# Optimization experiments

Measured on AMD Instinct MI355X. Metric: run time of the kernel, lower is better.

## Reference

```python
import jax, jax.numpy as jnp
import numpy as np

LMAX = 3
NBASIS = 10
MAX_RADIUS = 10.0
NUM_GRAPHS = 1024
N_NODES = 50000
Z_DIM = 16
SH_DIM = (LMAX + 1) ** 2  # 16
SMOOTH_FINITE_C = 1.14136  # e3nn normalization constant for smooth_finite basis


def spherical_harmonics_l3(vec):
    """e3nn real spherical harmonics, lmax=3, normalize=True, normalization='component'.
    vec: [N,3] -> [N,16]."""
    r = jnp.linalg.norm(vec, axis=-1, keepdims=True)
    u = vec / r
    x, y, z = u[..., 0], u[..., 1], u[..., 2]
    one = jnp.ones_like(x)
    s3, s5, s7, s15 = np.sqrt(3.0), np.sqrt(5.0), np.sqrt(7.0), np.sqrt(15.0)
    x2, y2, z2 = x * x, y * y, z * z
    x2z2 = x2 + z2
    # l = 2 (e3nn generated polynomials, component normalization)
    sh2_0 = s15 * x * z
    sh2_1 = s15 * x * y
    sh2_2 = s5 * (y2 - 0.5 * x2z2)
    sh2_3 = s15 * y * z
    sh2_4 = (s15 / 2.0) * (z2 - x2)
    # l = 3
    c42_6 = np.sqrt(42.0) / 6.0
    c168_8 = np.sqrt(168.0) / 8.0
    sh3_0 = c42_6 * (sh2_0 * z + sh2_4 * x)
    sh3_1 = s7 * sh2_0 * y
    sh3_2 = c168_8 * (4.0 * y2 - x2z2) * x
    sh3_3 = (s7 / 2.0) * y * (2.0 * y2 - 3.0 * x2z2)
    sh3_4 = c168_8 * z * (4.0 * y2 - x2z2)
    sh3_5 = s7 * sh2_4 * y
    sh3_6 = c42_6 * (sh2_4 * z - sh2_0 * x)
    return jnp.stack([
        one,
        s3 * x, s3 * y, s3 * z,
        sh2_0, sh2_1, sh2_2, sh2_3, sh2_4,
        sh3_0, sh3_1, sh3_2, sh3_3, sh3_4, sh3_5, sh3_6,
    ], axis=-1)


def soft_one_hot_smooth_finite(d):
    """e3nn soft_one_hot_linspace(basis='smooth_finite', cutoff=True). d: [N] -> [N, NBASIS]."""
    values = jnp.linspace(0.0, MAX_RADIUS, NBASIS + 2)[1:-1]  # interior points
    step = MAX_RADIUS / (NBASIS + 1)
    diff = (d[:, None] - values) / step

    def soft_unit_step(u):
        safe = jnp.where(u > 0.0, u, 1.0)
        return jnp.where(u > 0.0, jnp.exp(-1.0 / safe), 0.0)

    c = SMOOTH_FINITE_C * np.exp(2.0)
    return c * soft_unit_step(diff + 1.0) * soft_unit_step(1.0 - diff)


def setup_inputs() -> dict:
    key = jax.random.key(0)
    k1, k2, k3 = jax.random.split(key, 3)
    x = jax.random.uniform(k1, (N_NODES, Z_DIM), dtype=jnp.float32)
    pos = jax.random.normal(k2, (N_NODES, 3), dtype=jnp.float32)
    batch = jnp.sort(jax.random.randint(k3, (N_NODES,), 0, NUM_GRAPHS, dtype=jnp.int64))
    return {"x": x, "pos": pos, "batch": batch}


def reference(x, pos, batch):
    edge_vec = pos
    edge_length = jnp.linalg.norm(edge_vec, axis=1)
    # radial embedding, scaled by sqrt(number_of_basis)
    basis = soft_one_hot_smooth_finite(edge_length) * np.sqrt(NBASIS)  # [N, B]
    sh = spherical_harmonics_l3(edge_vec)  # [N, 16]
    # FullTensorProduct(Zx0e, sh) then FullTensorProduct(., Bx0e):
    # scalar x irrep paths reduce to exact elementwise products (component norm),
    # with e3nn layout per l-block: [z, b, m] flattened, blocks concatenated over l.
    n = x.shape[0]
    sh_slices = [(0, 1), (1, 4), (4, 9), (9, 16)]  # l = 0..3
    blocks = []
    for lo, hi in sh_slices:
        blk = jnp.einsum('nz,nb,nm->nzbm', x, basis, sh[:, lo:hi])
        blocks.append(blk.reshape(n, -1))
    feats = jnp.concatenate(blocks, axis=-1)  # [N, Z*B*16]
    # scatter mean over graphs
    seg_sum = jax.ops.segment_sum(feats, batch, num_segments=NUM_GRAPHS)
    cnt = jax.ops.segment_sum(jnp.ones((n, 1), dtype=feats.dtype), batch, num_segments=NUM_GRAPHS)
    return seg_sum / jnp.maximum(cnt, 1.0)
```

## Files before the change

kernel.cpp:

```cpp
#include <hip/hip_runtime.h>
#include <cmath>

#define NGRAPHS 1024
#define ZDIM 16
#define NB 10
#define SHD 16
#define FEAT 2560
#define CHUNK 96
#define CSTRIDE 132
#define WIN 1536

__global__ __launch_bounds__(256) void yfe_kernel(
    const float* __restrict__ xin,
    const float* __restrict__ pos,
    const int* __restrict__ batch,
    float* __restrict__ out,
    int n_nodes)
{
    const int g = blockIdx.x;
    const int tid = threadIdx.x;
    const int n = n_nodes;

    __shared__ int s_red[12];
    __shared__ int s_cnt[2][9];
    __shared__ __align__(16) float s_xT[ZDIM][CSTRIDE];
    __shared__ __align__(16) float s_shA[SHD][CSTRIDE];
    __shared__ __align__(16) float s_shB[SHD][CSTRIDE];
    __shared__ __align__(16) float s_out[FEAT];

    int start, end;
    bool window_ok = (n >= WIN);
    if (window_ok) {
        const int ctr = (int)(((long long)(2 * g + 1) * n) >> 11);
        int p0 = ctr - WIN / 2;
        if (p0 < 0) p0 = 0;
        if (p0 > n - WIN) p0 = n - WIN;
        int vals[6];
#pragma unroll
        for (int k = 0; k < 6; ++k) vals[k] = batch[p0 + tid + k * 256];
        int wA = 0, wB = 0;
#pragma unroll
        for (int k = 0; k < 6; ++k) {
            wA += __popcll(__ballot(vals[k] < g));
            wB += __popcll(__ballot(vals[k] < g + 1));
        }
        if ((tid & 63) == 0) {
            s_red[tid >> 6]       = wA;
            s_red[4 + (tid >> 6)] = wB;
        }
        if (tid == 0)   s_red[8] = vals[0];
        if (tid == 255) s_red[9] = vals[5];
        __syncthreads();
        const int KA = s_red[0] + s_red[1] + s_red[2] + s_red[3];
        const int KB = s_red[4] + s_red[5] + s_red[6] + s_red[7];
        start = p0 + KA;
        end   = p0 + KB;
        const bool left_ok  = (p0 == 0) || (s_red[8] < g);
        const bool right_ok = (p0 + WIN == n) || (s_red[9] >= g + 1);
        window_ok = left_ok && right_ok;
        __syncthreads();
    }
    if (!window_ok) {
        {
            const int pos1 = (int)(((long long)tid * n) >> 8);
            const int v = batch[pos1];
            const unsigned long long balA = __ballot(v < g);
            const unsigned long long balB = __ballot(v < g + 1);
            if ((tid & 63) == 0) {
                s_red[tid >> 6]       = __popcll(balA);
                s_red[4 + (tid >> 6)] = __popcll(balB);
            }
        }
        __syncthreads();
        const int KA = s_red[0] + s_red[1] + s_red[2] + s_red[3];
        const int KB = s_red[4] + s_red[5] + s_red[6] + s_red[7];
        const int loA = (KA == 0) ? 0 : (int)(((long long)(KA - 1) * n) >> 8) + 1;
        const int hiA = (KA == 256) ? n : (int)(((long long)KA * n) >> 8);
        const int loB = (KB == 0) ? 0 : (int)(((long long)(KB - 1) * n) >> 8) + 1;
        const int hiB = (KB == 256) ? n : (int)(((long long)KB * n) >> 8);
        __syncthreads();
        const int pA = loA + tid;
        const int pB = loB + tid;
        const int prA = (pA < hiA) ? (batch[pA] < g) : 0;
        const int prB = (pB < hiB) ? (batch[pB] < g + 1) : 0;
        const unsigned long long balA = __ballot(prA);
        const unsigned long long balB = __ballot(prB);
        if ((tid & 63) == 0) {
            s_red[tid >> 6]       = __popcll(balA);
            s_red[4 + (tid >> 6)] = __popcll(balB);
        }
        __syncthreads();
        start = loA + s_red[0] + s_red[1] + s_red[2] + s_red[3];
        end   = loB + s_red[4] + s_red[5] + s_red[6] + s_red[7];
        __syncthreads();
    }
    const int cnt = end - start;

    const int zi  = tid >> 4;
    const int shi = tid & 15;
    const int l   = (shi >= 9) ? 3 : (shi >= 4) ? 2 : (shi >= 1) ? 1 : 0;
    const int m   = shi - l * l;
    const int w   = 2 * l + 1;
    const int off = (l == 0) ? 0 : (l == 1) ? 160 : (l == 2) ? 640 : 1440;
    const int fbase = off + zi * 10 * w + m;

    float acc[NB];
#pragma unroll
    for (int b = 0; b < NB; ++b) acc[b] = 0.0f;

    const float CB = (float)(1.14136 * 7.389056098930650 * 3.1622776601683795);

    for (int nb0 = start; nb0 < end; nb0 += CHUNK) {
        const int nrem = min(CHUNK, end - nb0);
        __syncthreads();

        {
            const float4 z4 = make_float4(0.f, 0.f, 0.f, 0.f);
            float4* zx = (float4*)s_xT;
            float4* za = (float4*)s_shA;
            float4* zb = (float4*)s_shB;
            for (int i = tid; i < (ZDIM * CSTRIDE) / 4; i += 256) {
                zx[i] = z4; za[i] = z4; zb[i] = z4;
            }
        }

        int   my_ib = 9;
        int   my_rank = 0;
        float4 xr0, xr1, xr2, xr3;
        float sh[SHD];
        float bvA = 0.0f, bvB = 0.0f;
        if (tid < nrem) {
            const int node = nb0 + tid;
            const float4* xp = (const float4*)(xin + (size_t)node * ZDIM);
            xr0 = xp[0]; xr1 = xp[1]; xr2 = xp[2]; xr3 = xp[3];
            const float px = pos[node * 3 + 0];
            const float py = pos[node * 3 + 1];
            const float pz = pos[node * 3 + 2];
            const float r2 = px * px + py * py + pz * pz;
            const float rinv = rsqrtf(r2);
            const float X = px * rinv, Y = py * rinv, Z = pz * rinv;
            const float x2 = X * X, y2 = Y * Y, z2 = Z * Z;
            const float x2z2 = x2 + z2;
            const float s3  = 1.7320508075688772f;
            const float s5  = 2.2360679774997896f;
            const float s7  = 2.6457513110645907f;
            const float s15 = 3.8729833462074170f;
            const float c42_6  = 1.0801234497346435f;
            const float c168_8 = 1.6201851746019651f;
            const float sh2_0 = s15 * X * Z;
            const float sh2_1 = s15 * X * Y;
            const float sh2_2 = s5 * (y2 - 0.5f * x2z2);
            const float sh2_3 = s15 * Y * Z;
            const float sh2_4 = 0.5f * s15 * (z2 - x2);
            sh[0]  = 1.0f;
            sh[1]  = s3 * X;
            sh[2]  = s3 * Y;
            sh[3]  = s3 * Z;
            sh[4]  = sh2_0;
            sh[5]  = sh2_1;
            sh[6]  = sh2_2;
            sh[7]  = sh2_3;
            sh[8]  = sh2_4;
            sh[9]  = c42_6 * (sh2_0 * Z + sh2_4 * X);
            sh[10] = s7 * sh2_0 * Y;
            sh[11] = c168_8 * (4.0f * y2 - x2z2) * X;
            sh[12] = 0.5f * s7 * Y * (2.0f * y2 - 3.0f * x2z2);
            sh[13] = c168_8 * Z * (4.0f * y2 - x2z2);
            sh[14] = s7 * sh2_4 * Y;
            sh[15] = c42_6 * (sh2_4 * Z - sh2_0 * X);
            const float d = r2 * rinv;
            const float t = d * 1.1f;
            int ib = (int)floorf(t) - 1;
            ib = min(max(ib, 0), 8);
            {
                const float u1 = t - (float)ib, u2 = (float)(ib + 2) - t;
                if (u1 > 0.0f && u2 > 0.0f) bvA = CB * __expf(-1.0f / u1 - 1.0f / u2);
                const float v1 = t - (float)(ib + 1), v2 = (float)(ib + 3) - t;
                if (v1 > 0.0f && v2 > 0.0f) bvB = CB * __expf(-1.0f / v1 - 1.0f / v2);
            }
            my_ib = ib;
        }
        if (tid < 128) {
            const unsigned long long lt = (1ull << (unsigned)(tid & 63)) - 1ull;
#pragma unroll
            for (int v = 0; v < 9; ++v) {
                const unsigned long long bal = __ballot(my_ib == v);
                if (my_ib == v) my_rank = __popcll(bal & lt);
                if ((tid & 63) == 0) s_cnt[tid >> 6][v] = __popcll(bal);
            }
        }
        __syncthreads();

        int cum[10];
        {
            cum[0] = 0;
#pragma unroll
            for (int v = 0; v < 9; ++v)
                cum[v + 1] = cum[v] + ((s_cnt[0][v] + s_cnt[1][v] + 3) & ~3);
        }

        if (tid < nrem) {
            int dest = my_rank;
            if (tid >= 64) dest += s_cnt[0][my_ib];
#pragma unroll
            for (int v = 0; v < 9; ++v) {
                const int pv = (s_cnt[0][v] + s_cnt[1][v] + 3) & ~3;
                dest += (v < my_ib) ? pv : 0;
            }
#pragma unroll
            for (int k = 0; k < SHD; ++k) {
                s_shA[k][dest] = sh[k] * bvA;
                s_shB[k][dest] = sh[k] * bvB;
            }
            s_xT[ 0][dest] = xr0.x; s_xT[ 1][dest] = xr0.y;
            s_xT[ 2][dest] = xr0.z; s_xT[ 3][dest] = xr0.w;
            s_xT[ 4][dest] = xr1.x; s_xT[ 5][dest] = xr1.y;
            s_xT[ 6][dest] = xr1.z; s_xT[ 7][dest] = xr1.w;
            s_xT[ 8][dest] = xr2.x; s_xT[ 9][dest] = xr2.y;
            s_xT[10][dest] = xr2.z; s_xT[11][dest] = xr2.w;
            s_xT[12][dest] = xr3.x; s_xT[13][dest] = xr3.y;
            s_xT[14][dest] = xr3.z; s_xT[15][dest] = xr3.w;
        }
        __syncthreads();

#pragma unroll
        for (int v = 0; v < 9; ++v) {
            for (int c = cum[v]; c < cum[v + 1]; c += 4) {
                const float4 xv = *(const float4*)&s_xT[zi][c];
                const float4 sA = *(const float4*)&s_shA[shi][c];
                const float4 sB = *(const float4*)&s_shB[shi][c];
                acc[v] = fmaf(xv.w, sA.w, fmaf(xv.z, sA.z,
                         fmaf(xv.y, sA.y, fmaf(xv.x, sA.x, acc[v]))));
                acc[v + 1] = fmaf(xv.w, sB.w, fmaf(xv.z, sB.z,
                             fmaf(xv.y, sB.y, fmaf(xv.x, sB.x, acc[v + 1]))));
            }
        }
    }

    const float scale = 1.0f / (float)max(cnt, 1);
#pragma unroll
    for (int b = 0; b < NB; ++b) s_out[fbase + b * w] = acc[b] * scale;
    __syncthreads();
    float4* og4 = (float4*)(out + (size_t)g * FEAT);
    const float4* so4 = (const float4*)s_out;
    for (int i = tid; i < FEAT / 4; i += 256) og4[i] = so4[i];
}

extern "C" void kernel_launch(void* const* d_in, const int* in_sizes, int n_in,
                              void* d_out, int out_size, void* d_ws, size_t ws_size,
                              hipStream_t stream) {
    const float* x   = (const float*)d_in[0];
    const float* pos = (const float*)d_in[1];
    const int* batch = (const int*)d_in[2];
    float* out = (float*)d_out;
    const int n_nodes = in_sizes[2];

    hipLaunchKernelGGL(yfe_kernel, dim3(NGRAPHS), dim3(256), 0, stream,
                       x, pos, batch, out, n_nodes);
}
```

Measured before the change: 65.74 us.

## Split each graph's nodes across two 256-thread halves with separate staging buffers

Doubles the block to 512 threads. Each half processes half of the graph's node range with its own shared-memory staging buffers, and the two partial accumulators are combined through shared memory at the end. The per-chunk binning is done within a single wavefront using ballots, and only padding slots are zeroed instead of clearing the full buffers every chunk. This aims to raise the parallelism available per graph and cut sync and zeroing overhead, at the cost of larger blocks, an extra reduction step, and possibly lower occupancy.

```diff
diff --git a/kernel.cpp b/kernel.cpp
--- a/kernel.cpp
+++ b/kernel.cpp
@@ -6,11 +6,11 @@
 #define NB 10
 #define SHD 16
 #define FEAT 2560
-#define CHUNK 96
-#define CSTRIDE 132
+#define HCHUNK 64
+#define CSTRIDE 92
 #define WIN 1536
 
-__global__ __launch_bounds__(256) void yfe_kernel(
+__global__ __launch_bounds__(512) void yfe_kernel(
     const float* __restrict__ xin,
     const float* __restrict__ pos,
     const int* __restrict__ batch,
@@ -20,13 +20,18 @@
     const int g = blockIdx.x;
     const int tid = threadIdx.x;
     const int n = n_nodes;
-
-    __shared__ int s_red[12];
-    __shared__ int s_cnt[2][9];
-    __shared__ __align__(16) float s_xT[ZDIM][CSTRIDE];
-    __shared__ __align__(16) float s_shA[SHD][CSTRIDE];
-    __shared__ __align__(16) float s_shB[SHD][CSTRIDE];
-    __shared__ __align__(16) float s_out[FEAT];
+    const int h = tid >> 8;
+    const int t = tid & 255;
+
+    __shared__ int s_red[18];
+    __shared__ int s_cum[2][10];
+    __shared__ __align__(16) float s_stage[2][3][SHD][CSTRIDE];
+
+    {
+        const float4 z4 = make_float4(0.f, 0.f, 0.f, 0.f);
+        float4* z = (float4*)s_stage;
+        for (int i = tid; i < (int)(sizeof(s_stage) / 16); i += 512) z[i] = z4;
+    }
 
     int start, end;
     bool window_ok = (n >= WIN);
@@ -35,49 +40,51 @@
         int p0 = ctr - WIN / 2;
         if (p0 < 0) p0 = 0;
         if (p0 > n - WIN) p0 = n - WIN;
-        int vals[6];
-#pragma unroll
-        for (int k = 0; k < 6; ++k) vals[k] = batch[p0 + tid + k * 256];
+        int vals[3];
+#pragma unroll
+        for (int k = 0; k < 3; ++k) vals[k] = batch[p0 + tid + k * 512];
         int wA = 0, wB = 0;
 #pragma unroll
-        for (int k = 0; k < 6; ++k) {
+        for (int k = 0; k < 3; ++k) {
             wA += __popcll(__ballot(vals[k] < g));
             wB += __popcll(__ballot(vals[k] < g + 1));
         }
         if ((tid & 63) == 0) {
-            s_red[tid >> 6]       = wA;
-            s_red[4 + (tid >> 6)] = wB;
-        }
-        if (tid == 0)   s_red[8] = vals[0];
-        if (tid == 255) s_red[9] = vals[5];
-        __syncthreads();
-        const int KA = s_red[0] + s_red[1] + s_red[2] + s_red[3];
-        const int KB = s_red[4] + s_red[5] + s_red[6] + s_red[7];
+            s_red[tid >> 6]     = wA;
+            s_red[8 + (tid >> 6)] = wB;
+        }
+        if (tid == 0)   s_red[16] = vals[0];
+        if (tid == 511) s_red[17] = vals[2];
+        __syncthreads();
+        int KA = 0, KB = 0;
+#pragma unroll
+        for (int q = 0; q < 8; ++q) { KA += s_red[q]; KB += s_red[8 + q]; }
         start = p0 + KA;
         end   = p0 + KB;
-        const bool left_ok  = (p0 == 0) || (s_red[8] < g);
-        const bool right_ok = (p0 + WIN == n) || (s_red[9] >= g + 1);
+        const bool left_ok  = (p0 == 0) || (s_red[16] < g);
+        const bool right_ok = (p0 + WIN == n) || (s_red[17] >= g + 1);
         window_ok = left_ok && right_ok;
         __syncthreads();
     }
     if (!window_ok) {
         {
-            const int pos1 = (int)(((long long)tid * n) >> 8);
-            const int v = batch[pos1];
+            const int p1 = (int)(((long long)tid * n) >> 9);
+            const int v = batch[p1];
             const unsigned long long balA = __ballot(v < g);
             const unsigned long long balB = __ballot(v < g + 1);
             if ((tid & 63) == 0) {
                 s_red[tid >> 6]       = __popcll(balA);
-                s_red[4 + (tid >> 6)] = __popcll(balB);
-            }
-        }
-        __syncthreads();
-        const int KA = s_red[0] + s_red[1] + s_red[2] + s_red[3];
-        const int KB = s_red[4] + s_red[5] + s_red[6] + s_red[7];
-        const int loA = (KA == 0) ? 0 : (int)(((long long)(KA - 1) * n) >> 8) + 1;
-        const int hiA = (KA == 256) ? n : (int)(((long long)KA * n) >> 8);
-        const int loB = (KB == 0) ? 0 : (int)(((long long)(KB - 1) * n) >> 8) + 1;
-        const int hiB = (KB == 256) ? n : (int)(((long long)KB * n) >> 8);
+                s_red[8 + (tid >> 6)] = __popcll(balB);
+            }
+        }
+        __syncthreads();
+        int KA = 0, KB = 0;
+#pragma unroll
+        for (int q = 0; q < 8; ++q) { KA += s_red[q]; KB += s_red[8 + q]; }
+        const int loA = (KA == 0) ? 0 : (int)(((long long)(KA - 1) * n) >> 9) + 1;
+        const int hiA = (KA == 512) ? n : (int)(((long long)KA * n) >> 9);
+        const int loB = (KB == 0) ? 0 : (int)(((long long)(KB - 1) * n) >> 9) + 1;
+        const int hiB = (KB == 512) ? n : (int)(((long long)KB * n) >> 9);
         __syncthreads();
         const int pA = loA + tid;
         const int pB = loB + tid;
@@ -87,17 +94,28 @@
         const unsigned long long balB = __ballot(prB);
         if ((tid & 63) == 0) {
             s_red[tid >> 6]       = __popcll(balA);
-            s_red[4 + (tid >> 6)] = __popcll(balB);
-        }
-        __syncthreads();
-        start = loA + s_red[0] + s_red[1] + s_red[2] + s_red[3];
-        end   = loB + s_red[4] + s_red[5] + s_red[6] + s_red[7];
+            s_red[8 + (tid >> 6)] = __popcll(balB);
+        }
+        __syncthreads();
+        int sA = 0, sB = 0;
+#pragma unroll
+        for (int q = 0; q < 8; ++q) { sA += s_red[q]; sB += s_red[8 + q]; }
+        start = loA + sA;
+        end   = loB + sB;
         __syncthreads();
     }
     const int cnt = end - start;
-
-    const int zi  = tid >> 4;
-    const int shi = tid & 15;
+    const int mid = start + ((cnt + 1) >> 1);
+    const int hstart = h ? mid : start;
+    const int hend   = h ? end : mid;
+    const int nchunks = (((cnt + 1) >> 1) + HCHUNK - 1) >> 6;
+
+    float (*xT )[CSTRIDE] = s_stage[h][0];
+    float (*shA)[CSTRIDE] = s_stage[h][1];
+    float (*shB)[CSTRIDE] = s_stage[h][2];
+
+    const int zi  = t >> 4;
+    const int shi = t & 15;
     const int l   = (shi >= 9) ? 3 : (shi >= 4) ? 2 : (shi >= 1) ? 1 : 0;
     const int m   = shi - l * l;
     const int w   = 2 * l + 1;
@@ -110,125 +128,128 @@
 
     const float CB = (float)(1.14136 * 7.389056098930650 * 3.1622776601683795);
 
-    for (int nb0 = start; nb0 < end; nb0 += CHUNK) {
-        const int nrem = min(CHUNK, end - nb0);
-        __syncthreads();
-
-        {
-            const float4 z4 = make_float4(0.f, 0.f, 0.f, 0.f);
-            float4* zx = (float4*)s_xT;
-            float4* za = (float4*)s_shA;
-            float4* zb = (float4*)s_shB;
-            for (int i = tid; i < (ZDIM * CSTRIDE) / 4; i += 256) {
-                zx[i] = z4; za[i] = z4; zb[i] = z4;
-            }
-        }
-
-        int   my_ib = 9;
-        int   my_rank = 0;
-        float4 xr0, xr1, xr2, xr3;
-        float sh[SHD];
-        float bvA = 0.0f, bvB = 0.0f;
-        if (tid < nrem) {
-            const int node = nb0 + tid;
-            const float4* xp = (const float4*)(xin + (size_t)node * ZDIM);
-            xr0 = xp[0]; xr1 = xp[1]; xr2 = xp[2]; xr3 = xp[3];
-            const float px = pos[node * 3 + 0];
-            const float py = pos[node * 3 + 1];
-            const float pz = pos[node * 3 + 2];
-            const float r2 = px * px + py * py + pz * pz;
-            const float rinv = rsqrtf(r2);
-            const float X = px * rinv, Y = py * rinv, Z = pz * rinv;
-            const float x2 = X * X, y2 = Y * Y, z2 = Z * Z;
-            const float x2z2 = x2 + z2;
-            const float s3  = 1.7320508075688772f;
-            const float s5  = 2.2360679774997896f;
-            const float s7  = 2.6457513110645907f;
-            const float s15 = 3.8729833462074170f;
-            const float c42_6  = 1.0801234497346435f;
-            const float c168_8 = 1.6201851746019651f;
-            const float sh2_0 = s15 * X * Z;
-            const float sh2_1 = s15 * X * Y;
-            const float sh2_2 = s5 * (y2 - 0.5f * x2z2);
-            const float sh2_3 = s15 * Y * Z;
-            const float sh2_4 = 0.5f * s15 * (z2 - x2);
-            sh[0]  = 1.0f;
-            sh[1]  = s3 * X;
-            sh[2]  = s3 * Y;
-            sh[3]  = s3 * Z;
-            sh[4]  = sh2_0;
-            sh[5]  = sh2_1;
-            sh[6]  = sh2_2;
-            sh[7]  = sh2_3;
-            sh[8]  = sh2_4;
-            sh[9]  = c42_6 * (sh2_0 * Z + sh2_4 * X);
-            sh[10] = s7 * sh2_0 * Y;
-            sh[11] = c168_8 * (4.0f * y2 - x2z2) * X;
-            sh[12] = 0.5f * s7 * Y * (2.0f * y2 - 3.0f * x2z2);
-            sh[13] = c168_8 * Z * (4.0f * y2 - x2z2);
-            sh[14] = s7 * sh2_4 * Y;
-            sh[15] = c42_6 * (sh2_4 * Z - sh2_0 * X);
-            const float d = r2 * rinv;
-            const float t = d * 1.1f;
-            int ib = (int)floorf(t) - 1;
-            ib = min(max(ib, 0), 8);
-            {
-                const float u1 = t - (float)ib, u2 = (float)(ib + 2) - t;
-                if (u1 > 0.0f && u2 > 0.0f) bvA = CB * __expf(-1.0f / u1 - 1.0f / u2);
-                const float v1 = t - (float)(ib + 1), v2 = (float)(ib + 3) - t;
-                if (v1 > 0.0f && v2 > 0.0f) bvB = CB * __expf(-1.0f / v1 - 1.0f / v2);
-            }
-            my_ib = ib;
-        }
-        if (tid < 128) {
-            const unsigned long long lt = (1ull << (unsigned)(tid & 63)) - 1ull;
+    for (int ic = 0; ic < nchunks; ++ic) {
+        const int nb0 = hstart + (ic << 6);
+        int nrem = hend - nb0;
+        nrem = (nrem < 0) ? 0 : ((nrem > HCHUNK) ? HCHUNK : nrem);
+        __syncthreads();
+
+        if (t < 64) {
+            int my_ib = 9;
+            float bvA = 0.0f, bvB = 0.0f;
+            float sh[SHD];
+            float4 xr0, xr1, xr2, xr3;
+            if (t < nrem) {
+                const int node = nb0 + t;
+                const float px = pos[node * 3 + 0];
+                const float py = pos[node * 3 + 1];
+                const float pz = pos[node * 3 + 2];
+                const float4* xp = (const float4*)(xin + (size_t)node * ZDIM);
+                xr0 = xp[0]; xr1 = xp[1]; xr2 = xp[2]; xr3 = xp[3];
+                const float r2 = px * px + py * py + pz * pz;
+                const float rinv = rsqrtf(r2);
+                const float X = px * rinv, Y = py * rinv, Z = pz * rinv;
+                const float x2 = X * X, y2 = Y * Y, z2 = Z * Z;
+                const float x2z2 = x2 + z2;
+                const float s3  = 1.7320508075688772f;
+                const float s5  = 2.2360679774997896f;
+                const float s7  = 2.6457513110645907f;
+                const float s15 = 3.8729833462074170f;
+                const float c42_6  = 1.0801234497346435f;
+                const float c168_8 = 1.6201851746019651f;
+                const float sh2_0 = s15 * X * Z;
+                const float sh2_1 = s15 * X * Y;
+                const float sh2_2 = s5 * (y2 - 0.5f * x2z2);
+                const float sh2_3 = s15 * Y * Z;
+                const float sh2_4 = 0.5f * s15 * (z2 - x2);
+                sh[0]  = 1.0f;
+                sh[1]  = s3 * X;
+                sh[2]  = s3 * Y;
+                sh[3]  = s3 * Z;
+                sh[4]  = sh2_0;
+                sh[5]  = sh2_1;
+                sh[6]  = sh2_2;
+                sh[7]  = sh2_3;
+                sh[8]  = sh2_4;
+                sh[9]  = c42_6 * (sh2_0 * Z + sh2_4 * X);
+                sh[10] = s7 * sh2_0 * Y;
+                sh[11] = c168_8 * (4.0f * y2 - x2z2) * X;
+                sh[12] = 0.5f * s7 * Y * (2.0f * y2 - 3.0f * x2z2);
+                sh[13] = c168_8 * Z * (4.0f * y2 - x2z2);
+                sh[14] = s7 * sh2_4 * Y;
+                sh[15] = c42_6 * (sh2_4 * Z - sh2_0 * X);
+                const float d = r2 * rinv;
+                const float tt = d * 1.1f;
+                int ib = (int)floorf(tt) - 1;
+                ib = min(max(ib, 0), 8);
+                {
+                    const float u1 = tt - (float)ib, u2 = (float)(ib + 2) - tt;
+                    if (u1 > 0.0f && u2 > 0.0f) bvA = CB * __expf(-1.0f / u1 - 1.0f / u2);
+                    const float v1 = tt - (float)(ib + 1), v2 = (float)(ib + 3) - tt;
+                    if (v1 > 0.0f && v2 > 0.0f) bvB = CB * __expf(-1.0f / v1 - 1.0f / v2);
+                }
+                my_ib = ib;
+            }
+            const unsigned long long lt = (1ull << (unsigned)t) - 1ull;
+            int rank = 0, cv[9];
 #pragma unroll
             for (int v = 0; v < 9; ++v) {
                 const unsigned long long bal = __ballot(my_ib == v);
-                if (my_ib == v) my_rank = __popcll(bal & lt);
-                if ((tid & 63) == 0) s_cnt[tid >> 6][v] = __popcll(bal);
+                if (my_ib == v) rank = __popcll(bal & lt);
+                cv[v] = __popcll(bal);
+            }
+            int cum[10];
+            cum[0] = 0;
+#pragma unroll
+            for (int v = 0; v < 9; ++v) cum[v + 1] = cum[v] + ((cv[v] + 3) & ~3);
+#pragma unroll
+            for (int v = 0; v < 9; ++v) {
+                const int base = cum[v] + cv[v];
+                const int pe   = cum[v + 1];
+                for (int c = base + (t >> 5); c < pe; c += 2) {
+                    if (((t >> 4) & 1) == 0) shA[t & 15][c] = 0.0f;
+                    else                     shB[t & 15][c] = 0.0f;
+                }
+            }
+            if (t < nrem) {
+                int dest = rank;
+#pragma unroll
+                for (int v = 0; v < 9; ++v)
+                    dest += (v < my_ib) ? ((cv[v] + 3) & ~3) : 0;
+#pragma unroll
+                for (int k = 0; k < SHD; ++k) {
+                    shA[k][dest] = sh[k] * bvA;
+                    shB[k][dest] = sh[k] * bvB;
+                }
+                xT[ 0][dest] = xr0.x; xT[ 1][dest] = xr0.y;
+                xT[ 2][dest] = xr0.z; xT[ 3][dest] = xr0.w;
+                xT[ 4][dest] = xr1.x; xT[ 5][dest] = xr1.y;
+                xT[ 6][dest] = xr1.z; xT[ 7][dest] = xr1.w;
+                xT[ 8][dest] = xr2.x; xT[ 9][dest] = xr2.y;
+                xT[10][dest] = xr2.z; xT[11][dest] = xr2.w;
+                xT[12][dest] = xr3.x; xT[13][dest] = xr3.y;
+                xT[14][dest] = xr3.z; xT[15][dest] = xr3.w;
+            }
+            if (t == 0) {
+                s_cum[h][0] = cum[0]; s_cum[h][1] = cum[1]; s_cum[h][2] = cum[2];
+                s_cum[h][3] = cum[3]; s_cum[h][4] = cum[4]; s_cum[h][5] = cum[5];
+                s_cum[h][6] = cum[6]; s_cum[h][7] = cum[7]; s_cum[h][8] = cum[8];
+                s_cum[h][9] = cum[9];
             }
         }
         __syncthreads();
 
         int cum[10];
-        {
-            cum[0] = 0;
-#pragma unroll
-            for (int v = 0; v < 9; ++v)
-                cum[v + 1] = cum[v] + ((s_cnt[0][v] + s_cnt[1][v] + 3) & ~3);
-        }
-
-        if (tid < nrem) {
-            int dest = my_rank;
-            if (tid >= 64) dest += s_cnt[0][my_ib];
-#pragma unroll
-            for (int v = 0; v < 9; ++v) {
-                const int pv = (s_cnt[0][v] + s_cnt[1][v] + 3) & ~3;
-                dest += (v < my_ib) ? pv : 0;
-            }
-#pragma unroll
-            for (int k = 0; k < SHD; ++k) {
-                s_shA[k][dest] = sh[k] * bvA;
-                s_shB[k][dest] = sh[k] * bvB;
-            }
-            s_xT[ 0][dest] = xr0.x; s_xT[ 1][dest] = xr0.y;
-            s_xT[ 2][dest] = xr0.z; s_xT[ 3][dest] = xr0.w;
-            s_xT[ 4][dest] = xr1.x; s_xT[ 5][dest] = xr1.y;
-            s_xT[ 6][dest] = xr1.z; s_xT[ 7][dest] = xr1.w;
-            s_xT[ 8][dest] = xr2.x; s_xT[ 9][dest] = xr2.y;
-            s_xT[10][dest] = xr2.z; s_xT[11][dest] = xr2.w;
-            s_xT[12][dest] = xr3.x; s_xT[13][dest] = xr3.y;
-            s_xT[14][dest] = xr3.z; s_xT[15][dest] = xr3.w;
-        }
-        __syncthreads();
+#pragma unroll
+        for (int v = 0; v < 10; ++v) cum[v] = s_cum[h][v];
 
 #pragma unroll
         for (int v = 0; v < 9; ++v) {
+#pragma unroll 2
             for (int c = cum[v]; c < cum[v + 1]; c += 4) {
-                const float4 xv = *(const float4*)&s_xT[zi][c];
-                const float4 sA = *(const float4*)&s_shA[shi][c];
-                const float4 sB = *(const float4*)&s_shB[shi][c];
+                const float4 xv = *(const float4*)&xT[zi][c];
+                const float4 sA = *(const float4*)&shA[shi][c];
+                const float4 sB = *(const float4*)&shB[shi][c];
                 acc[v] = fmaf(xv.w, sA.w, fmaf(xv.z, sA.z,
                          fmaf(xv.y, sA.y, fmaf(xv.x, sA.x, acc[v]))));
                 acc[v + 1] = fmaf(xv.w, sB.w, fmaf(xv.z, sB.z,
@@ -237,13 +258,24 @@
         }
     }
 
+    __syncthreads();
     const float scale = 1.0f / (float)max(cnt, 1);
-#pragma unroll
-    for (int b = 0; b < NB; ++b) s_out[fbase + b * w] = acc[b] * scale;
+    float* comb = &s_stage[1][0][0][0];
+    if (h == 1) {
+#pragma unroll
+        for (int b = 0; b < NB; ++b) comb[fbase + b * w] = acc[b];
+    }
+    __syncthreads();
+    float* outbuf = &s_stage[0][0][0][0];
+    if (h == 0) {
+#pragma unroll
+        for (int b = 0; b < NB; ++b)
+            outbuf[fbase + b * w] = (acc[b] + comb[fbase + b * w]) * scale;
+    }
     __syncthreads();
     float4* og4 = (float4*)(out + (size_t)g * FEAT);
-    const float4* so4 = (const float4*)s_out;
-    for (int i = tid; i < FEAT / 4; i += 256) og4[i] = so4[i];
+    const float4* ob4 = (const float4*)outbuf;
+    for (int i = tid; i < FEAT / 4; i += 512) og4[i] = ob4[i];
 }
 
 extern "C" void kernel_launch(void* const* d_in, const int* in_sizes, int n_in,
@@ -255,6 +287,6 @@
     float* out = (float*)d_out;
     const int n_nodes = in_sizes[2];
 
-    hipLaunchKernelGGL(yfe_kernel, dim3(NGRAPHS), dim3(256), 0, stream,
+    hipLaunchKernelGGL(yfe_kernel, dim3(NGRAPHS), dim3(512), 0, stream,
                        x, pos, batch, out, n_nodes);
 }
```

Result: slower. 72.44 us (+10.2%).
